# Optimization experiments

Measured on AMD Instinct MI355X. Metric: run time of the kernel, lower is better.

Reference implementation:

```python
import jax, jax.numpy as jnp
import numpy as np

# Hard-concrete gate constants (module defaults)
TEMP = 2.0 / 3.0          # gate_temperature
STRETCH_EPS = 0.1         # gate_stretch_epsilon -> stretch to [-0.1, 1.1]
PRE_CLIP = 2.0            # gate_pre_activation_clip

N_NODES = 100000
N_CLUSTERS = 32
N_RELATIONS = 8
N_EDGES = 500000


def _hard_concrete_gate_eval(log_alpha):
    # eval-mode sample: deterministic, pre = log_alpha / temperature
    pre = jnp.clip(log_alpha / TEMP, -PRE_CLIP, PRE_CLIP)
    lo, hi = -STRETCH_EPS, 1.0 + STRETCH_EPS
    z = jax.nn.sigmoid(pre) * (hi - lo) + lo
    return jnp.clip(z, 0.0, 1.0)


def setup_inputs() -> dict:
    key = jax.random.key(0)
    k0, k1, k2, k3, k4, k5 = jax.random.split(key, 6)
    assignments = jax.random.normal(k0, (N_NODES, N_CLUSTERS), dtype=jnp.float32)
    edge_index = jax.random.randint(k1, (2, N_EDGES), 0, N_NODES, dtype=jnp.int64)
    edge_type = jax.random.randint(k2, (N_EDGES,), 0, N_RELATIONS, dtype=jnp.int64)
    inter_cluster_logits = jax.random.normal(k3, (N_RELATIONS, N_CLUSTERS, N_CLUSTERS), dtype=jnp.float32)
    gate_log_alpha = jax.random.normal(k4, (N_RELATIONS, N_CLUSTERS, N_CLUSTERS), dtype=jnp.float32)
    absent_bias = jax.random.normal(k5, (N_RELATIONS,), dtype=jnp.float32) * 0.1
    return {
        "assignments": assignments,
        "edge_index": edge_index,
        "edge_type": edge_type,
        "inter_cluster_logits": inter_cluster_logits,
        "gate_log_alpha": gate_log_alpha,
        "absent_bias": absent_bias,
    }


def reference(assignments, edge_index, edge_type, inter_cluster_logits, gate_log_alpha, absent_bias):
    # weights = sigmoid(logits) * hard_concrete_gate(log_alpha)   [R, K, K]
    weights = jax.nn.sigmoid(inter_cluster_logits) * _hard_concrete_gate_eval(gate_log_alpha)
    src = assignments[edge_index[0]]   # [E, K]
    dst = assignments[edge_index[1]]   # [E, K]
    # weighted_dst[e] = weights[edge_type[e]] @ dst[e]
    # compute all-relation products then gather (avoids materializing [E,K,K])
    wd_all = jnp.einsum('ej,rij->eri', dst, weights)            # [E, R, K]
    weighted_dst = jnp.take_along_axis(wd_all, edge_type[:, None, None], axis=1)[:, 0, :]  # [E, K]
    logits = jnp.sum(src * weighted_dst, axis=-1) + absent_bias[edge_type]  # [E]
    return logits
```

## Files before the change

### kernel.cpp

```cpp
#include <hip/hip_runtime.h>
#include <hip/hip_bf16.h>
#include <cstdint>

#define KDIM 32
#define RMAX 8
#define NBLK 256

typedef _Float16 half2v __attribute__((ext_vector_type(2)));

__device__ __forceinline__ float sigmoidf_(float x) {
    return 1.0f / (1.0f + expf(-x));
}

__device__ __forceinline__ float gate_weight_(float logit, float log_alpha) {
    float pre = log_alpha * 1.5f;
    pre = fminf(fmaxf(pre, -2.0f), 2.0f);
    float z = sigmoidf_(pre) * 1.2f - 0.1f;
    z = fminf(fmaxf(z, 0.0f), 1.0f);
    return sigmoidf_(logit) * z;
}

__global__ __launch_bounds__(256) void prep_kernel(
    const int* __restrict__ et, int E, int chunk,
    int* __restrict__ bh , int R,
    const float* __restrict__ logits, const float* __restrict__ la,
    _Float16* __restrict__ Wh, int n,
    const float* __restrict__ A, _Float16* __restrict__ Ah, int nA) {
    int g = blockIdx.x * blockDim.x + threadIdx.x;
    if (g < n) Wh[g] = (_Float16)gate_weight_(logits[g], la[g]);

    int nthreads = gridDim.x * blockDim.x;
    int n4 = nA >> 2;
    for (int i4 = g; i4 < n4; i4 += nthreads) {
        float4 v = ((const float4*)A)[i4];
        half2v h0; h0[0] = (_Float16)v.x; h0[1] = (_Float16)v.y;
        half2v h1; h1[0] = (_Float16)v.z; h1[1] = (_Float16)v.w;
        ((half2v*)Ah)[i4 * 2 + 0] = h0;
        ((half2v*)Ah)[i4 * 2 + 1] = h1;
    }

    __shared__ int h[RMAX];
    if ((int)threadIdx.x < RMAX) h[threadIdx.x] = 0;
    __syncthreads();
    int b = blockIdx.x;
    int start = b * chunk;
    int end = start + chunk;
    if (end > E) end = E;
    for (int i = start + threadIdx.x; i < end; i += blockDim.x) {
        atomicAdd(&h[et[i]], 1);
    }
    __syncthreads();
    if ((int)threadIdx.x < RMAX) bh[b * RMAX + threadIdx.x] = h[threadIdx.x];
}

__global__ __launch_bounds__(512) void scan2_kernel(
    int* __restrict__ bh, int* __restrict__ off,
    int4* __restrict__ edata, int R) {
    __shared__ int tr[RMAX][NBLK];
    __shared__ int cnt_s[RMAX];
    __shared__ int off_s[RMAX + 1];
    int t = threadIdx.x;

    for (int i = t; i < NBLK * RMAX; i += 512) {
        int b = i / RMAX, r = i % RMAX;
        tr[r][b] = bh[i];
    }
    __syncthreads();

    int w = t >> 6;
    int lane = t & 63;
    if (w < R) {
        int b0 = lane * 4;
        int v0 = tr[w][b0 + 0];
        int v1 = tr[w][b0 + 1];
        int v2 = tr[w][b0 + 2];
        int v3 = tr[w][b0 + 3];
        int s0 = v0, s1 = s0 + v1, s2 = s1 + v2, s3 = s2 + v3;
        int lanesum = s3;
        int sc = lanesum;
#pragma unroll
        for (int d = 1; d < 64; d <<= 1) {
            int up = __shfl_up(sc, d, 64);
            if (lane >= d) sc += up;
        }
        int excl = sc - lanesum;
        tr[w][b0 + 0] = excl;
        tr[w][b0 + 1] = excl + s0;
        tr[w][b0 + 2] = excl + s1;
        tr[w][b0 + 3] = excl + s2;
        if (lane == 63) cnt_s[w] = sc;
    }
    __syncthreads();

    if (t == 0) {
        int o = 0;
        off_s[0] = 0;
        for (int r = 0; r < R; r++) {
            o += (cnt_s[r] + 63) & ~63;
            off_s[r + 1] = o;
        }
        for (int r = 0; r <= R; r++) off[r] = off_s[r];
    }
    __syncthreads();

    for (int i = t; i < NBLK * RMAX; i += 512) {
        int b = i / RMAX, r = i % RMAX;
        bh[i] = tr[r][b] + ((r < R) ? off_s[r] : 0);
    }
    for (int r = 0; r < R; r++) {
        int padStart = off_s[r] + cnt_s[r];
        int padEnd = off_s[r + 1];
        for (int i = padStart + t; i < padEnd; i += 512) {
            edata[i] = make_int4(0, 0, -1, 0);
        }
    }
}

__global__ __launch_bounds__(256) void scatter3_kernel(
    const int* __restrict__ et, const int* __restrict__ ei, int E, int chunk,
    const int* __restrict__ bh, int4* __restrict__ edata, int R) {
    __shared__ int cur[RMAX];
    int b = blockIdx.x;
    if ((int)threadIdx.x < RMAX) cur[threadIdx.x] = bh[b * RMAX + threadIdx.x];
    __syncthreads();
    int start = b * chunk;
    int end = start + chunk;
    if (end > E) end = E;
    for (int i = start + threadIdx.x; i < end; i += blockDim.x) {
        int r = et[i];
        int sn = ei[i];
        int dn = ei[E + i];
        int pos = atomicAdd(&cur[r], 1);
        edata[pos] = make_int4(sn, dn, i, 0);
    }
}

__global__ __launch_bounds__(256) void gather3_kernel(
    const _Float16* __restrict__ Ah, const _Float16* __restrict__ Wh,
    const float* __restrict__ bias, const int4* __restrict__ edata,
    const int* __restrict__ off, float* __restrict__ out, int cap, int R) {
    int g = blockIdx.x * blockDim.x + threadIdx.x;
    if (g >= cap) return;

    int r = 0;
    for (int rr = 1; rr < R; rr++) r += (g >= off[rr]) ? 1 : 0;
    r = __builtin_amdgcn_readfirstlane(r);

    int4 rec = edata[g];
    bool valid = (rec.z >= 0);
    int sn = valid ? rec.x : 0;
    int dn = valid ? rec.y : 0;

    const uint4* As = (const uint4*)(Ah + (size_t)sn * KDIM);
    const uint4* Ad = (const uint4*)(Ah + (size_t)dn * KDIM);
    unsigned int sp[16], dp[16];
#pragma unroll
    for (int q = 0; q < 4; q++) {
        uint4 s4 = As[q];
        uint4 d4 = Ad[q];
        sp[4 * q + 0] = s4.x; sp[4 * q + 1] = s4.y;
        sp[4 * q + 2] = s4.z; sp[4 * q + 3] = s4.w;
        dp[4 * q + 0] = d4.x; dp[4 * q + 1] = d4.y;
        dp[4 * q + 2] = d4.z; dp[4 * q + 3] = d4.w;
    }

    const unsigned int* __restrict__ Wr =
        (const unsigned int*)(Wh + (size_t)r * (KDIM * KDIM));
    float total = 0.0f;
#pragma unroll
    for (int i = 0; i < KDIM; i++) {
        float acc = 0.0f;
#pragma unroll
        for (int j2 = 0; j2 < KDIM / 2; j2++) {
            half2v w = __builtin_bit_cast(half2v, Wr[i * 16 + j2]);
            half2v d = __builtin_bit_cast(half2v, dp[j2]);
#if __has_builtin(__builtin_amdgcn_fdot2)
            acc = __builtin_amdgcn_fdot2(w, d, acc, false);
#else
            acc = fmaf((float)w[0], (float)d[0], acc);
            acc = fmaf((float)w[1], (float)d[1], acc);
#endif
        }
        half2v s2 = __builtin_bit_cast(half2v, sp[i >> 1]);
        float sv = (float)s2[i & 1];
        total = fmaf(sv, acc, total);
    }

    if (valid) out[rec.z] = total + bias[r];
}

__global__ __launch_bounds__(256) void gather_unsorted_kernel(
    const float* __restrict__ A, const int* __restrict__ ei,
    const int* __restrict__ et,
    const float* __restrict__ logits, const float* __restrict__ la,
    const float* __restrict__ bias, float* __restrict__ out, int E, int R) {
    __shared__ float Wl[RMAX * 1032];
    int total_w = R * KDIM * KDIM;
    for (int t = threadIdx.x; t < total_w; t += blockDim.x) {
        int r = t / (KDIM * KDIM);
        int ij = t % (KDIM * KDIM);
        Wl[r * 1032 + ij] = gate_weight_(logits[t], la[t]);
    }
    __syncthreads();

    for (int e = blockIdx.x * blockDim.x + threadIdx.x; e < E;
         e += gridDim.x * blockDim.x) {
        int r = et[e];
        int sn = ei[e];
        int dn = ei[E + e];
        const float4* As = (const float4*)(A + (size_t)sn * KDIM);
        const float4* Ad = (const float4*)(A + (size_t)dn * KDIM);
        float sv[KDIM], dv[KDIM];
#pragma unroll
        for (int q = 0; q < KDIM / 4; q++) {
            float4 s4 = As[q];
            float4 d4 = Ad[q];
            sv[4 * q + 0] = s4.x; sv[4 * q + 1] = s4.y;
            sv[4 * q + 2] = s4.z; sv[4 * q + 3] = s4.w;
            dv[4 * q + 0] = d4.x; dv[4 * q + 1] = d4.y;
            dv[4 * q + 2] = d4.z; dv[4 * q + 3] = d4.w;
        }
        float totalv = 0.0f;
#pragma unroll
        for (int i = 0; i < KDIM; i++) {
            const float* Wrow = &Wl[r * 1032 + i * KDIM];
            float acc = 0.0f;
#pragma unroll
            for (int j = 0; j < KDIM / 4; j++) {
                float4 w4 = ((const float4*)Wrow)[j];
                acc = fmaf(w4.x, dv[4 * j + 0], acc);
                acc = fmaf(w4.y, dv[4 * j + 1], acc);
                acc = fmaf(w4.z, dv[4 * j + 2], acc);
                acc = fmaf(w4.w, dv[4 * j + 3], acc);
            }
            totalv = fmaf(sv[i], acc, totalv);
        }
        out[e] = totalv + bias[r];
    }
}

extern "C" void kernel_launch(void* const* d_in, const int* in_sizes, int n_in,
                              void* d_out, int out_size, void* d_ws, size_t ws_size,
                              hipStream_t stream) {
    const float* A      = (const float*)d_in[0];
    const int*   ei     = (const int*)d_in[1];
    const int*   et     = (const int*)d_in[2];
    const float* logits = (const float*)d_in[3];
    const float* la     = (const float*)d_in[4];
    const float* bias   = (const float*)d_in[5];
    float* out = (float*)d_out;

    int E = in_sizes[2];
    int R = in_sizes[5];
    int n = in_sizes[3];
    int nA = in_sizes[0];

    int cap = E + 64 * RMAX;
    size_t ahb = ((size_t)nA * 2 + 15) & ~(size_t)15;
    size_t edata_off = 16384 + 64 + (size_t)NBLK * RMAX * 4 + ahb;
    size_t need = edata_off + (size_t)cap * 16;

    if (R <= RMAX && ws_size >= need) {
        char* ws = (char*)d_ws;
        _Float16* Wh = (_Float16*)(ws);
        int* off     = (int*)(ws + 16384);
        int* bh      = (int*)(ws + 16384 + 64);
        _Float16* Ah = (_Float16*)(ws + 16384 + 64 + NBLK * RMAX * 4);
        int4* edata  = (int4*)(ws + edata_off);

        int chunk = (E + NBLK - 1) / NBLK;

        prep_kernel<<<NBLK, 256, 0, stream>>>(
            et, E, chunk, bh, R, logits, la, Wh, n, A, Ah, nA);
        scan2_kernel<<<1, 512, 0, stream>>>(bh, off, edata, R);
        scatter3_kernel<<<NBLK, 256, 0, stream>>>(et, ei, E, chunk, bh, edata, R);
        gather3_kernel<<<(cap + 255) / 256, 256, 0, stream>>>(
            Ah, Wh, bias, edata, off, out, cap, R);
    } else {
        int gblocks = (E + 255) / 256;
        if (gblocks > 2048) gblocks = 2048;
        gather_unsorted_kernel<<<gblocks, 256, 0, stream>>>(
            A, ei, et, logits, la, bias, out, E, R);
    }
}
```

Baseline: 108.1 us.

## Compute per-edge bilinear form with MFMA 16x16x16 f16 matrix instructions

Replaces the per-thread fdot2 bilinear evaluation with a wave-level MFMA scheme. Each wave processes 16 edges at a time: it computes W·dst with four MFMAs, converts the result to fp16, then computes src·(W·dst) with two more MFMAs and reads only the diagonal entries. This is meant to move the 32x32 matrix-vector work off the vector ALUs onto the matrix cores. In exchange, it adds an intermediate fp16 rounding and wastes most of the second MFMA's output. The workspace capacity is also rounded up to a multiple of 256 so whole waves always index valid records.

```diff
diff --git a/kernel.cpp b/kernel.cpp
--- a/kernel.cpp
+++ b/kernel.cpp
@@ -7,6 +7,14 @@
 #define NBLK 256
 
 typedef _Float16 half2v __attribute__((ext_vector_type(2)));
+typedef _Float16 half4v __attribute__((ext_vector_type(4)));
+typedef float    f32x4  __attribute__((ext_vector_type(4)));
+
+#if __has_builtin(__builtin_amdgcn_mfma_f32_16x16x16f16)
+#define USE_MFMA 1
+#else
+#define USE_MFMA 0
+#endif
 
 __device__ __forceinline__ float sigmoidf_(float x) {
     return 1.0f / (1.0f + expf(-x));
@@ -135,12 +143,79 @@
     }
 }
 
-__global__ __launch_bounds__(256) void gather3_kernel(
+#if USE_MFMA
+__global__ __launch_bounds__(256) void gather4_kernel(
     const _Float16* __restrict__ Ah, const _Float16* __restrict__ Wh,
     const float* __restrict__ bias, const int4* __restrict__ edata,
-    const int* __restrict__ off, float* __restrict__ out, int cap, int R) {
+    const int* __restrict__ off, float* __restrict__ out, int capA, int R) {
     int g = blockIdx.x * blockDim.x + threadIdx.x;
-    if (g >= cap) return;
+    int lane = threadIdx.x & 63;
+    int lm = lane & 15;
+    int lg = lane >> 4;
+    int kq = lg * 4;
+
+    int r = 0;
+    for (int rr = 1; rr < R; rr++) r += (g >= off[rr]) ? 1 : 0;
+    r = __builtin_amdgcn_readfirstlane(r);
+    float br = bias[r];
+
+    const _Float16* Wr = Wh + (size_t)r * (KDIM * KDIM);
+    half4v aw1 = *(const half4v*)(Wr + lm * KDIM + kq);
+    half4v aw2 = *(const half4v*)(Wr + lm * KDIM + 16 + kq);
+    half4v aw3 = *(const half4v*)(Wr + (16 + lm) * KDIM + kq);
+    half4v aw4 = *(const half4v*)(Wr + (16 + lm) * KDIM + 16 + kq);
+
+    int wbase = (blockIdx.x * blockDim.x + (threadIdx.x & ~63));
+    f32x4 zeroF = {0.0f, 0.0f, 0.0f, 0.0f};
+    bool diag_lane = (lg == (lm >> 2));
+
+#pragma unroll
+    for (int s = 0; s < 4; s++) {
+        int4 rec = edata[wbase + s * 16 + lm];
+        bool valid = (rec.z >= 0);
+        int sn = valid ? rec.x : 0;
+        int dn = valid ? rec.y : 0;
+
+        const _Float16* Sp = Ah + (size_t)sn * KDIM;
+        const _Float16* Dp = Ah + (size_t)dn * KDIM;
+        half4v as1 = *(const half4v*)(Sp + kq);
+        half4v as2 = *(const half4v*)(Sp + 16 + kq);
+        half4v bd1 = *(const half4v*)(Dp + kq);
+        half4v bd2 = *(const half4v*)(Dp + 16 + kq);
+
+        f32x4 z1 = __builtin_amdgcn_mfma_f32_16x16x16f16(aw1, bd1, zeroF, 0, 0, 0);
+        z1 = __builtin_amdgcn_mfma_f32_16x16x16f16(aw2, bd2, z1, 0, 0, 0);
+        f32x4 z2 = __builtin_amdgcn_mfma_f32_16x16x16f16(aw3, bd1, zeroF, 0, 0, 0);
+        z2 = __builtin_amdgcn_mfma_f32_16x16x16f16(aw4, bd2, z2, 0, 0, 0);
+
+        half4v zb1, zb2;
+#if __has_builtin(__builtin_amdgcn_cvt_pkrtz)
+        half2v t0 = __builtin_bit_cast(half2v, __builtin_amdgcn_cvt_pkrtz(z1[0], z1[1]));
+        half2v t1 = __builtin_bit_cast(half2v, __builtin_amdgcn_cvt_pkrtz(z1[2], z1[3]));
+        half2v t2 = __builtin_bit_cast(half2v, __builtin_amdgcn_cvt_pkrtz(z2[0], z2[1]));
+        half2v t3 = __builtin_bit_cast(half2v, __builtin_amdgcn_cvt_pkrtz(z2[2], z2[3]));
+        zb1[0] = t0[0]; zb1[1] = t0[1]; zb1[2] = t1[0]; zb1[3] = t1[1];
+        zb2[0] = t2[0]; zb2[1] = t2[1]; zb2[2] = t3[0]; zb2[3] = t3[1];
+#else
+        zb1[0] = (_Float16)z1[0]; zb1[1] = (_Float16)z1[1];
+        zb1[2] = (_Float16)z1[2]; zb1[3] = (_Float16)z1[3];
+        zb2[0] = (_Float16)z2[0]; zb2[1] = (_Float16)z2[1];
+        zb2[2] = (_Float16)z2[2]; zb2[3] = (_Float16)z2[3];
+#endif
+
+        f32x4 c = __builtin_amdgcn_mfma_f32_16x16x16f16(as1, zb1, zeroF, 0, 0, 0);
+        c = __builtin_amdgcn_mfma_f32_16x16x16f16(as2, zb2, c, 0, 0, 0);
+
+        if (valid && diag_lane) out[rec.z] = c[lm & 3] + br;
+    }
+}
+#else
+__global__ __launch_bounds__(256) void gather4_kernel(
+    const _Float16* __restrict__ Ah, const _Float16* __restrict__ Wh,
+    const float* __restrict__ bias, const int4* __restrict__ edata,
+    const int* __restrict__ off, float* __restrict__ out, int capA, int R) {
+    int g = blockIdx.x * blockDim.x + threadIdx.x;
+    if (g >= capA) return;
 
     int r = 0;
     for (int rr = 1; rr < R; rr++) r += (g >= off[rr]) ? 1 : 0;
@@ -188,6 +263,7 @@
 
     if (valid) out[rec.z] = total + bias[r];
 }
+#endif
 
 __global__ __launch_bounds__(256) void gather_unsorted_kernel(
     const float* __restrict__ A, const int* __restrict__ ei,
@@ -255,10 +331,10 @@
     int n = in_sizes[3];
     int nA = in_sizes[0];
 
-    int cap = E + 64 * RMAX;
+    int capA = (E + 64 * RMAX + 255) & ~255;
     size_t ahb = ((size_t)nA * 2 + 15) & ~(size_t)15;
     size_t edata_off = 16384 + 64 + (size_t)NBLK * RMAX * 4 + ahb;
-    size_t need = edata_off + (size_t)cap * 16;
+    size_t need = edata_off + (size_t)capA * 16;
 
     if (R <= RMAX && ws_size >= need) {
         char* ws = (char*)d_ws;
@@ -274,8 +350,8 @@
             et, E, chunk, bh, R, logits, la, Wh, n, A, Ah, nA);
         scan2_kernel<<<1, 512, 0, stream>>>(bh, off, edata, R);
         scatter3_kernel<<<NBLK, 256, 0, stream>>>(et, ei, E, chunk, bh, edata, R);
-        gather3_kernel<<<(cap + 255) / 256, 256, 0, stream>>>(
-            Ah, Wh, bias, edata, off, out, cap, R);
+        gather4_kernel<<<capA / 256, 256, 0, stream>>>(
+            Ah, Wh, bias, edata, off, out, capA, R);
     } else {
         int gblocks = (E + 255) / 256;
         if (gblocks > 2048) gblocks = 2048;
```

Measured after the change: 106.0 us. 2.0% less time.
